# Optimization experiments

Measured on AMD Instinct MI355X. Metric: run time of the kernel, lower is better.

Reference implementation:

```python
import jax, jax.numpy as jnp
import numpy as np

DIM = 768
HEADS = 12
MLP_DIM = 3072
EPS = 1e-5


def setup_inputs() -> dict:
    key = jax.random.key(0)
    ks = jax.random.split(key, 10)
    s = lambda d: 1.0 / np.sqrt(d)
    return {
        "x": jax.random.normal(ks[0], (8, 1024, DIM), dtype=jnp.float32),
        "ln1_g": jnp.ones((DIM,), jnp.float32),
        "ln1_b": jnp.zeros((DIM,), jnp.float32),
        "w_qkv": jax.random.normal(ks[1], (DIM, 3 * DIM), jnp.float32) * s(DIM),
        "w_out": jax.random.normal(ks[2], (DIM, DIM), jnp.float32) * s(DIM),
        "b_out": jnp.zeros((DIM,), jnp.float32),
        "ln2_g": jnp.ones((DIM,), jnp.float32),
        "ln2_b": jnp.zeros((DIM,), jnp.float32),
        "w1": jax.random.normal(ks[3], (DIM, MLP_DIM), jnp.float32) * s(DIM),
        "b1": jnp.zeros((MLP_DIM,), jnp.float32),
        "w2": jax.random.normal(ks[4], (MLP_DIM, DIM), jnp.float32) * s(MLP_DIM),
        "b2": jnp.zeros((DIM,), jnp.float32),
    }


def _layernorm(x, g, b):
    mu = jnp.mean(x, axis=-1, keepdims=True)
    var = jnp.mean(jnp.square(x - mu), axis=-1, keepdims=True)
    return (x - mu) * jax.lax.rsqrt(var + EPS) * g + b


def _block(x, ln1_g, ln1_b, w_qkv, w_out, b_out, ln2_g, ln2_b, w1, b1, w2, b2):
    B, N, C = x.shape
    H = HEADS
    Dh = C // H
    scale = Dh ** -0.5
    # attention
    h = _layernorm(x, ln1_g, ln1_b)
    qkv = (h @ w_qkv).reshape(B, N, 3, H, Dh)
    q, k, v = qkv[:, :, 0], qkv[:, :, 1], qkv[:, :, 2]  # [B,N,H,Dh]
    attn = jnp.einsum("bnhd,bmhd->bhnm", q, k) * scale
    attn = jax.nn.softmax(attn, axis=-1)
    o = jnp.einsum("bhnm,bmhd->bnhd", attn, v).reshape(B, N, C)
    x = x + o @ w_out + b_out
    # mlp (exact erf GELU, matching torch nn.GELU default)
    h = _layernorm(x, ln2_g, ln2_b)
    h = jax.nn.gelu(h @ w1 + b1, approximate=False)
    x = x + h @ w2 + b2
    return x


def reference(x, ln1_g, ln1_b, w_qkv, w_out, b_out, ln2_g, ln2_b, w1, b1, w2, b2):
    return _block(x, ln1_g, ln1_b, w_qkv, w_out, b_out, ln2_g, ln2_b, w1, b1, w2, b2)
```

## Files before the change

### kernel.cpp

```cpp
#include <hip/hip_runtime.h>
#include <hip/hip_bf16.h>
#include <cstdint>

#define DIM 768
#define HEADS 12
#define DH 64
#define MLP_DIM 3072
#define ROWS 8192
#define SEQ 1024
#define PPAD 72

typedef __attribute__((ext_vector_type(8))) short bf16x8;
typedef __attribute__((ext_vector_type(4))) float f32x4;

typedef __attribute__((address_space(1))) void GV;
typedef __attribute__((address_space(3))) void SV;

__device__ inline void async16(const void* g, void* l) {
  __builtin_amdgcn_global_load_lds((GV*)(void*)g, (SV*)l, 16, 0, 0);
}

__device__ inline unsigned short f2b(float f) {
  union { float f; uint32_t u; } v; v.f = f;
  uint32_t u = v.u;
  return (unsigned short)((u + 0x7fffu + ((u >> 16) & 1u)) >> 16);
}

__device__ inline float gelu_f(float v) {
  float x = v * 0.70710678118654752f;
  float ax = fabsf(x);
  float t = 1.f / (1.f + 0.47047f * ax);
  float poly = t * (0.3480242f + t * (-0.0958798f + t * 0.7478556f));
  float erfv = 1.f - poly * __expf(-ax * ax);
  erfv = copysignf(erfv, x);
  return 0.5f * v * (1.f + erfv);
}

__global__ __launch_bounds__(256) void transpose_k(const float* __restrict__ in,
                                                   unsigned short* __restrict__ out,
                                                   int K, int N) {
  __shared__ float t[32][33];
  int tx = threadIdx.x & 31, ty = threadIdx.x >> 5;
  int bn = blockIdx.x * 32, bk = blockIdx.y * 32;
#pragma unroll
  for (int i = ty; i < 32; i += 8) t[i][tx] = in[(size_t)(bk + i) * N + bn + tx];
  __syncthreads();
#pragma unroll
  for (int i = ty; i < 32; i += 8) out[(size_t)(bn + i) * K + bk + tx] = f2b(t[tx][i]);
}

__global__ __launch_bounds__(256) void ln_k(const float* __restrict__ x,
                                            const float* __restrict__ g,
                                            const float* __restrict__ b,
                                            unsigned short* __restrict__ h) {
  int wave = threadIdx.x >> 6, lane = threadIdx.x & 63;
  int row = blockIdx.x * 4 + wave;
  const float4* xr = (const float4*)(x + (size_t)row * DIM);
  float4 v[3];
  float s = 0.f;
#pragma unroll
  for (int j = 0; j < 3; ++j) {
    v[j] = xr[lane + j * 64];
    s += (v[j].x + v[j].y) + (v[j].z + v[j].w);
  }
#pragma unroll
  for (int m = 1; m < 64; m <<= 1) s += __shfl_xor(s, m);
  float mu = s * (1.f / DIM);
  float vs = 0.f;
#pragma unroll
  for (int j = 0; j < 3; ++j) {
    float d0 = v[j].x - mu, d1 = v[j].y - mu, d2 = v[j].z - mu, d3 = v[j].w - mu;
    vs += (d0 * d0 + d1 * d1) + (d2 * d2 + d3 * d3);
  }
#pragma unroll
  for (int m = 1; m < 64; m <<= 1) vs += __shfl_xor(vs, m);
  float rstd = rsqrtf(vs * (1.f / DIM) + 1e-5f);
  const float4* g4 = (const float4*)g;
  const float4* b4 = (const float4*)b;
  unsigned short* hr = h + (size_t)row * DIM;
#pragma unroll
  for (int j = 0; j < 3; ++j) {
    int i = lane + j * 64;
    float4 gg = g4[i], bb = b4[i];
    float y0 = (v[j].x - mu) * rstd * gg.x + bb.x;
    float y1 = (v[j].y - mu) * rstd * gg.y + bb.y;
    float y2 = (v[j].z - mu) * rstd * gg.z + bb.z;
    float y3 = (v[j].w - mu) * rstd * gg.w + bb.w;
    uint2 pk;
    pk.x = (uint32_t)f2b(y0) | ((uint32_t)f2b(y1) << 16);
    pk.y = (uint32_t)f2b(y2) | ((uint32_t)f2b(y3) << 16);
    *(uint2*)(hr + i * 4) = pk;
  }
}

template <int MODE, int TM>
__global__ __launch_bounds__(256, 3) void gemm_k(
    const unsigned short* __restrict__ A, const unsigned short* __restrict__ Bt,
    int M, int N, int K,
    const float* __restrict__ bias, const float* __restrict__ resid,
    float* __restrict__ outf, unsigned short* __restrict__ outb) {
  constexpr int MI = (TM == 128) ? 4 : 2;
  __shared__ __align__(16) unsigned short As[2][TM * 64];
  __shared__ __align__(16) unsigned short Bs[2][128 * 64];
  int tid = threadIdx.x;
  int wave = tid >> 6, lane = tid & 63, lrow = lane & 15, qd = lane >> 4;
  int ntn = N >> 7;

  int nwg = gridDim.x;
  int wg = blockIdx.x;
  if ((nwg & 7) == 0) wg = (wg & 7) * (nwg >> 3) + (wg >> 3);

  int bm = (wg / ntn) * TM;
  int bn = (wg % ntn) << 7;
  int wm = (TM == 128) ? (wave >> 1) * 64 : (wave & 1) * 32;
  int wn = (TM == 128) ? (wave & 1) * 64 : (wave >> 1) * 64;

  f32x4 acc[MI][4];
#pragma unroll
  for (int i = 0; i < MI; ++i)
#pragma unroll
    for (int j = 0; j < 4; ++j) acc[i][j] = (f32x4){0.f, 0.f, 0.f, 0.f};

  int srow = tid >> 3;
  int c = (tid & 7) ^ (srow & 7);
  const char* gA = (const char*)(A + (size_t)(bm + srow) * K) + c * 16;
  const char* gB = (const char*)(Bt + (size_t)(bn + srow) * K) + c * 16;
  size_t rstep = (size_t)32 * K * 2;

  auto stage = [&](int kt, int buf) {
    size_t ko = (size_t)kt * 128;
    char* lA = (char*)(As[buf]) + tid * 16;
    char* lB = (char*)(Bs[buf]) + tid * 16;
#pragma unroll
    for (int j = 0; j < TM / 32; ++j) async16(gA + ko + j * rstep, lA + j * 4096);
#pragma unroll
    for (int j = 0; j < 4; ++j) async16(gB + ko + j * rstep, lB + j * 4096);
  };

  int nk = K >> 6;
  stage(0, 0);
  for (int kt = 0; kt < nk; ++kt) {
    asm volatile("s_waitcnt vmcnt(0)" ::: "memory");
    __syncthreads();
    if (kt + 1 < nk) stage(kt + 1, (kt + 1) & 1);
    const unsigned short* Asb = As[kt & 1];
    const unsigned short* Bsb = Bs[kt & 1];
#pragma unroll
    for (int s = 0; s < 2; ++s) {
      int q = s * 4 + qd;
      bf16x8 af[MI], bfr[4];
#pragma unroll
      for (int i = 0; i < MI; ++i) {
        int r = wm + i * 16 + lrow;
        af[i] = *(const bf16x8*)(Asb + r * 64 + ((q ^ (r & 7)) << 3));
      }
#pragma unroll
      for (int i = 0; i < 4; ++i) {
        int r = wn + i * 16 + lrow;
        bfr[i] = *(const bf16x8*)(Bsb + r * 64 + ((q ^ (r & 7)) << 3));
      }
#pragma unroll
      for (int mi = 0; mi < MI; ++mi)
#pragma unroll
        for (int ni = 0; ni < 4; ++ni)
          acc[mi][ni] = __builtin_amdgcn_mfma_f32_16x16x32_bf16(af[mi], bfr[ni], acc[mi][ni], 0, 0, 0);
    }
  }

#pragma unroll
  for (int mi = 0; mi < MI; ++mi)
#pragma unroll
    for (int ni = 0; ni < 4; ++ni)
#pragma unroll
      for (int r = 0; r < 4; ++r) {
        int row = bm + wm + mi * 16 + qd * 4 + r;
        int col = bn + wn + ni * 16 + lrow;
        float v = acc[mi][ni][r];
        if (MODE == 1) {
          v += bias[col] + resid[(size_t)row * 768 + col];
          outf[(size_t)row * 768 + col] = v;
        } else {
          v += bias[col];
          outb[(size_t)row * MLP_DIM + col] = f2b(gelu_f(v));
        }
      }
}

template <int MODE>
__global__ __launch_bounds__(256, 3) void gemm1b_k(
    const unsigned short* __restrict__ A, const unsigned short* __restrict__ Bt,
    int M, int N, int K,
    const float* __restrict__ bias,
    unsigned short* __restrict__ outb,
    unsigned short* __restrict__ Qb, unsigned short* __restrict__ Kb,
    unsigned short* __restrict__ Vt) {
  __shared__ __align__(16) unsigned short As[128 * 64];
  __shared__ __align__(16) unsigned short Bs[128 * 64];
  int tid = threadIdx.x;
  int wave = tid >> 6, lane = tid & 63, lrow = lane & 15, qd = lane >> 4;
  int ntn = N >> 7;

  int nwg = gridDim.x;
  int wg = blockIdx.x;
  if ((nwg & 7) == 0) wg = (wg & 7) * (nwg >> 3) + (wg >> 3);

  int bm = (wg / ntn) << 7;
  int bn = (wg % ntn) << 7;
  int wm = (wave >> 1) * 64;
  int wn = (wave & 1) * 64;

  f32x4 acc[4][4];
#pragma unroll
  for (int i = 0; i < 4; ++i)
#pragma unroll
    for (int j = 0; j < 4; ++j) acc[i][j] = (f32x4){0.f, 0.f, 0.f, 0.f};

  int srow = tid >> 3;
  int c = (tid & 7) ^ (srow & 7);
  const char* gA = (const char*)(A + (size_t)(bm + srow) * K) + c * 16;
  const char* gB = (const char*)(Bt + (size_t)(bn + srow) * K) + c * 16;
  size_t rstep = (size_t)32 * K * 2;

  auto stage = [&](int kt) {
    size_t ko = (size_t)kt * 128;
    char* lA = (char*)As + tid * 16;
    char* lB = (char*)Bs + tid * 16;
#pragma unroll
    for (int j = 0; j < 4; ++j) async16(gA + ko + j * rstep, lA + j * 4096);
#pragma unroll
    for (int j = 0; j < 4; ++j) async16(gB + ko + j * rstep, lB + j * 4096);
  };

  int nk = K >> 6;
  stage(0);
  for (int kt = 0; kt < nk; ++kt) {
    __syncthreads();
#pragma unroll
    for (int s = 0; s < 2; ++s) {
      int q = s * 4 + qd;
      bf16x8 af[4], bfr[4];
#pragma unroll
      for (int i = 0; i < 4; ++i) {
        int r = wm + i * 16 + lrow;
        af[i] = *(const bf16x8*)(As + r * 64 + ((q ^ (r & 7)) << 3));
      }
#pragma unroll
      for (int i = 0; i < 4; ++i) {
        int r = wn + i * 16 + lrow;
        bfr[i] = *(const bf16x8*)(Bs + r * 64 + ((q ^ (r & 7)) << 3));
      }
#pragma unroll
      for (int mi = 0; mi < 4; ++mi)
#pragma unroll
        for (int ni = 0; ni < 4; ++ni)
          acc[mi][ni] = __builtin_amdgcn_mfma_f32_16x16x32_bf16(af[mi], bfr[ni], acc[mi][ni], 0, 0, 0);
    }
    __syncthreads();
    if (kt + 1 < nk) stage(kt + 1);
  }

#pragma unroll
  for (int mi = 0; mi < 4; ++mi)
#pragma unroll
    for (int ni = 0; ni < 4; ++ni)
#pragma unroll
      for (int r = 0; r < 4; ++r) {
        int row = bm + wm + mi * 16 + qd * 4 + r;
        int col = bn + wn + ni * 16 + lrow;
        float v = acc[mi][ni][r];
        if (MODE == 0) {
          int which = col / 768;
          int rem = col - which * 768;
          int hh = rem >> 6, dh = rem & 63;
          int bb = row >> 10, n = row & 1023;
          size_t bh = (size_t)(bb * HEADS + hh);
          if (which == 0) {
            Qb[(bh * SEQ + n) * DH + dh] = f2b(v * 0.125f);
          } else if (which == 1) {
            Kb[(bh * SEQ + n) * DH + (((dh >> 3) ^ (n & 7)) << 3) + (dh & 7)] = f2b(v);
          } else {
            Vt[(bh * DH + dh) * SEQ + (n & ~63) +
               ((((n >> 3) & 7) ^ (dh & 7)) << 3) + (n & 7)] = f2b(v);
          }
        } else {
          v += bias[col];
          outb[(size_t)row * MLP_DIM + col] = f2b(gelu_f(v));
        }
      }
}

__global__ __launch_bounds__(256, 3) void attn_k(const unsigned short* __restrict__ Qb,
                                                 const unsigned short* __restrict__ Kb,
                                                 const unsigned short* __restrict__ Vt,
                                                 unsigned short* __restrict__ o) {
  __shared__ __align__(16) unsigned short Ks[2][64 * 64];
  __shared__ __align__(16) unsigned short Vs[2][64 * 64];
  __shared__ __align__(16) unsigned short Pa[4][32 * PPAD];
  int tid = threadIdx.x;
  int wave = tid >> 6, lane = tid & 63;
  int lrow = lane & 15, qd = lane >> 4;
  int bh = blockIdx.x % 96;
  int qt = blockIdx.x / 96;
  int b = bh / HEADS, hh = bh % HEADS;
  const unsigned short* Qh = Qb + (size_t)bh * SEQ * DH;
  const char* Kh = (const char*)(Kb + (size_t)bh * SEQ * DH);
  const char* Vh = (const char*)(Vt + (size_t)bh * DH * SEQ);
  int qw = qt * 128 + wave * 32;

  bf16x8 qf[2][2];
#pragma unroll
  for (int qs = 0; qs < 2; ++qs)
#pragma unroll
    for (int hf = 0; hf < 2; ++hf)
      qf[qs][hf] = *(const bf16x8*)(Qh + (qw + qs * 16 + lrow) * DH + hf * 32 + qd * 8);

  f32x4 oacc[2][4];
#pragma unroll
  for (int qs = 0; qs < 2; ++qs)
#pragma unroll
    for (int d = 0; d < 4; ++d) oacc[qs][d] = (f32x4){0.f, 0.f, 0.f, 0.f};
  float li[2] = {0.f, 0.f};
  unsigned short* Pw = Pa[wave];

  auto stage = [&](int t, int buf) {
    const char* kbase = Kh + (size_t)t * 8192;
    char* kd = (char*)Ks[buf];
    async16(kbase + tid * 16, kd + tid * 16);
    async16(kbase + 4096 + tid * 16, kd + 4096 + tid * 16);
    const char* vbase = Vh + (size_t)t * 128;
    char* vd = (char*)Vs[buf];
    async16(vbase + (size_t)(tid >> 3) * 2048 + (tid & 7) * 16, vd + tid * 16);
    async16(vbase + (size_t)((tid >> 3) + 32) * 2048 + (tid & 7) * 16, vd + 4096 + tid * 16);
  };

  stage(0, 0);
  for (int t = 0; t < 16; ++t) {
    asm volatile("s_waitcnt vmcnt(0)" ::: "memory");
    __syncthreads();
    if (t < 15) stage(t + 1, (t + 1) & 1);
    const unsigned short* Kst = Ks[t & 1];
    const unsigned short* Vst = Vs[t & 1];

    f32x4 st[4][2];
#pragma unroll
    for (int kt = 0; kt < 4; ++kt) {
      int krow = kt * 16 + lrow;
      int ksw = krow & 7;
      const unsigned short* Kr = Kst + krow * 64;
      bf16x8 k0 = *(const bf16x8*)(Kr + ((qd ^ ksw) << 3));
      bf16x8 k1 = *(const bf16x8*)(Kr + (((qd + 4) ^ ksw) << 3));
#pragma unroll
      for (int qs = 0; qs < 2; ++qs) {
        f32x4 z = (f32x4){0.f, 0.f, 0.f, 0.f};
        z = __builtin_amdgcn_mfma_f32_16x16x32_bf16(k0, qf[qs][0], z, 0, 0, 0);
        z = __builtin_amdgcn_mfma_f32_16x16x32_bf16(k1, qf[qs][1], z, 0, 0, 0);
        st[kt][qs] = z;
      }
    }

#pragma unroll
    for (int kt = 0; kt < 4; ++kt)
#pragma unroll
      for (int qs = 0; qs < 2; ++qs) {
        float p0 = __expf(st[kt][qs][0]);
        float p1 = __expf(st[kt][qs][1]);
        float p2 = __expf(st[kt][qs][2]);
        float p3 = __expf(st[kt][qs][3]);
        li[qs] += (p0 + p1) + (p2 + p3);
        uint2 pk;
        pk.x = (uint32_t)f2b(p0) | ((uint32_t)f2b(p1) << 16);
        pk.y = (uint32_t)f2b(p2) | ((uint32_t)f2b(p3) << 16);
        *(uint2*)(Pw + (qs * 16 + lrow) * PPAD + kt * 16 + qd * 4) = pk;
      }
    asm volatile("s_waitcnt lgkmcnt(0)" ::: "memory");

    bf16x8 ap[2][2];
#pragma unroll
    for (int qs = 0; qs < 2; ++qs)
#pragma unroll
      for (int kh = 0; kh < 2; ++kh)
        ap[qs][kh] = *(const bf16x8*)(Pw + (qs * 16 + lrow) * PPAD + kh * 32 + qd * 8);

#pragma unroll
    for (int ds = 0; ds < 4; ++ds) {
      int vrow = ds * 16 + lrow;
      int vsw = vrow & 7;
      const unsigned short* Vr = Vst + vrow * 64;
      bf16x8 v0 = *(const bf16x8*)(Vr + ((qd ^ vsw) << 3));
      bf16x8 v1 = *(const bf16x8*)(Vr + (((4 + qd) ^ vsw) << 3));
#pragma unroll
      for (int qs = 0; qs < 2; ++qs) {
        oacc[qs][ds] = __builtin_amdgcn_mfma_f32_16x16x32_bf16(ap[qs][0], v0, oacc[qs][ds], 0, 0, 0);
        oacc[qs][ds] = __builtin_amdgcn_mfma_f32_16x16x32_bf16(ap[qs][1], v1, oacc[qs][ds], 0, 0, 0);
      }
    }
  }

#pragma unroll
  for (int qs = 0; qs < 2; ++qs) {
    li[qs] += __shfl_xor(li[qs], 16);
    li[qs] += __shfl_xor(li[qs], 32);
  }

#pragma unroll
  for (int qs = 0; qs < 2; ++qs)
#pragma unroll
    for (int r = 0; r < 4; ++r) {
      float inv = 1.f / __shfl(li[qs], qd * 4 + r);
      int n = qw + qs * 16 + qd * 4 + r;
#pragma unroll
      for (int ds = 0; ds < 4; ++ds) {
        int dh = ds * 16 + lrow;
        o[((size_t)(b * SEQ + n)) * DIM + hh * DH + dh] = f2b(oacc[qs][ds][r] * inv);
      }
    }
}

extern "C" void kernel_launch(void* const* d_in, const int* in_sizes, int n_in,
                              void* d_out, int out_size, void* d_ws, size_t ws_size,
                              hipStream_t stream) {
  const float* x     = (const float*)d_in[0];
  const float* ln1_g = (const float*)d_in[1];
  const float* ln1_b = (const float*)d_in[2];
  const float* w_qkv = (const float*)d_in[3];
  const float* w_out = (const float*)d_in[4];
  const float* b_out = (const float*)d_in[5];
  const float* ln2_g = (const float*)d_in[6];
  const float* ln2_b = (const float*)d_in[7];
  const float* w1    = (const float*)d_in[8];
  const float* b1    = (const float*)d_in[9];
  const float* w2    = (const float*)d_in[10];
  const float* b2    = (const float*)d_in[11];

  char* ws = (char*)d_ws;
  unsigned short* wqkvT = (unsigned short*)(ws + 0);
  unsigned short* woutT = (unsigned short*)(ws + 3538944);
  unsigned short* w1T   = (unsigned short*)(ws + 4718592);
  unsigned short* w2T   = (unsigned short*)(ws + 9437184);
  float*          x2    = (float*)(ws + 14155776);
  unsigned short* h     = (unsigned short*)(ws + 39321600);
  char* big = ws + 51904512;
  unsigned short* Qb = (unsigned short*)(big);
  unsigned short* Kb = (unsigned short*)(big + 12582912);
  unsigned short* Vt = (unsigned short*)(big + 25165824);
  unsigned short* ob = (unsigned short*)(big + 37748736);
  unsigned short* am = (unsigned short*)(big);

  transpose_k<<<dim3(72, 24), 256, 0, stream>>>(w_qkv, wqkvT, 768, 2304);
  transpose_k<<<dim3(24, 24), 256, 0, stream>>>(w_out, woutT, 768, 768);
  transpose_k<<<dim3(96, 24), 256, 0, stream>>>(w1, w1T, 768, 3072);
  transpose_k<<<dim3(24, 96), 256, 0, stream>>>(w2, w2T, 3072, 768);

  ln_k<<<2048, 256, 0, stream>>>(x, ln1_g, ln1_b, h);
  gemm1b_k<0><<<64 * 18, 256, 0, stream>>>(h, wqkvT, ROWS, 2304, 768,
                                           nullptr, nullptr, Qb, Kb, Vt);
  attn_k<<<768, 256, 0, stream>>>(Qb, Kb, Vt, ob);
  gemm_k<1, 64><<<128 * 6, 256, 0, stream>>>(ob, woutT, ROWS, 768, 768,
                                             b_out, x, x2, nullptr);
  ln_k<<<2048, 256, 0, stream>>>(x2, ln2_g, ln2_b, h);
  gemm1b_k<2><<<64 * 24, 256, 0, stream>>>(h, w1T, ROWS, 3072, 768,
                                           b1, am, nullptr, nullptr, nullptr);
  gemm_k<1, 64><<<128 * 6, 256, 0, stream>>>(am, w2T, ROWS, 768, 3072,
                                             b2, x2, (float*)d_out, nullptr);
}
```

Before: 356.9 us.

## Use 8-wave 256x128 GEMM tiles and single-buffered 128x64 tiles for projections

The QKV and MLP-up GEMMs move to a 512-thread kernel with 256x128 output tiles, so each B tile is reused across more rows. The N=768 GEMMs (out-proj, MLP-down) change from double-buffered 64x128 tiles to single-buffered 128x64 tiles with occupancy hint 4. Dropping double buffering gives up load/compute overlap inside a workgroup in exchange for less LDS and more resident workgroups. The larger tiles also mean fewer workgroups per GEMM, which may hurt wave balance across CUs.

```diff
diff --git a/kernel.cpp b/kernel.cpp
--- a/kernel.cpp
+++ b/kernel.cpp
@@ -93,33 +93,35 @@
   }
 }
 
-template <int MODE, int TM>
-__global__ __launch_bounds__(256, 3) void gemm_k(
+template <int MODE, int BN>
+__global__ __launch_bounds__(256, 4) void gemm1b_k(
     const unsigned short* __restrict__ A, const unsigned short* __restrict__ Bt,
     int M, int N, int K,
     const float* __restrict__ bias, const float* __restrict__ resid,
-    float* __restrict__ outf, unsigned short* __restrict__ outb) {
-  constexpr int MI = (TM == 128) ? 4 : 2;
-  __shared__ __align__(16) unsigned short As[2][TM * 64];
-  __shared__ __align__(16) unsigned short Bs[2][128 * 64];
+    float* __restrict__ outf, unsigned short* __restrict__ outb,
+    unsigned short* __restrict__ Qb, unsigned short* __restrict__ Kb,
+    unsigned short* __restrict__ Vt) {
+  constexpr int NI = BN / 32;
+  __shared__ __align__(16) unsigned short As[128 * 64];
+  __shared__ __align__(16) unsigned short Bs[BN * 64];
   int tid = threadIdx.x;
   int wave = tid >> 6, lane = tid & 63, lrow = lane & 15, qd = lane >> 4;
-  int ntn = N >> 7;
+  int ntn = N / BN;
 
   int nwg = gridDim.x;
   int wg = blockIdx.x;
   if ((nwg & 7) == 0) wg = (wg & 7) * (nwg >> 3) + (wg >> 3);
 
-  int bm = (wg / ntn) * TM;
-  int bn = (wg % ntn) << 7;
-  int wm = (TM == 128) ? (wave >> 1) * 64 : (wave & 1) * 32;
-  int wn = (TM == 128) ? (wave & 1) * 64 : (wave >> 1) * 64;
-
-  f32x4 acc[MI][4];
-#pragma unroll
-  for (int i = 0; i < MI; ++i)
-#pragma unroll
-    for (int j = 0; j < 4; ++j) acc[i][j] = (f32x4){0.f, 0.f, 0.f, 0.f};
+  int bm = (wg / ntn) << 7;
+  int bn = (wg % ntn) * BN;
+  int wm = (wave >> 1) * 64;
+  int wn = (wave & 1) * (BN / 2);
+
+  f32x4 acc[4][NI];
+#pragma unroll
+  for (int i = 0; i < 4; ++i)
+#pragma unroll
+    for (int j = 0; j < NI; ++j) acc[i][j] = (f32x4){0.f, 0.f, 0.f, 0.f};
 
   int srow = tid >> 3;
   int c = (tid & 7) ^ (srow & 7);
@@ -127,50 +129,48 @@
   const char* gB = (const char*)(Bt + (size_t)(bn + srow) * K) + c * 16;
   size_t rstep = (size_t)32 * K * 2;
 
-  auto stage = [&](int kt, int buf) {
+  auto stage = [&](int kt) {
     size_t ko = (size_t)kt * 128;
-    char* lA = (char*)(As[buf]) + tid * 16;
-    char* lB = (char*)(Bs[buf]) + tid * 16;
-#pragma unroll
-    for (int j = 0; j < TM / 32; ++j) async16(gA + ko + j * rstep, lA + j * 4096);
-#pragma unroll
-    for (int j = 0; j < 4; ++j) async16(gB + ko + j * rstep, lB + j * 4096);
+    char* lA = (char*)As + tid * 16;
+    char* lB = (char*)Bs + tid * 16;
+#pragma unroll
+    for (int j = 0; j < 4; ++j) async16(gA + ko + j * rstep, lA + j * 4096);
+#pragma unroll
+    for (int j = 0; j < BN / 32; ++j) async16(gB + ko + j * rstep, lB + j * 4096);
   };
 
   int nk = K >> 6;
-  stage(0, 0);
+  stage(0);
   for (int kt = 0; kt < nk; ++kt) {
-    asm volatile("s_waitcnt vmcnt(0)" ::: "memory");
     __syncthreads();
-    if (kt + 1 < nk) stage(kt + 1, (kt + 1) & 1);
-    const unsigned short* Asb = As[kt & 1];
-    const unsigned short* Bsb = Bs[kt & 1];
 #pragma unroll
     for (int s = 0; s < 2; ++s) {
       int q = s * 4 + qd;
-      bf16x8 af[MI], bfr[4];
-#pragma unroll
-      for (int i = 0; i < MI; ++i) {
+      bf16x8 af[4], bfr[NI];
+#pragma unroll
+      for (int i = 0; i < 4; ++i) {
         int r = wm + i * 16 + lrow;
-        af[i] = *(const bf16x8*)(Asb + r * 64 + ((q ^ (r & 7)) << 3));
-      }
-#pragma unroll
-      for (int i = 0; i < 4; ++i) {
+        af[i] = *(const bf16x8*)(As + r * 64 + ((q ^ (r & 7)) << 3));
+      }
+#pragma unroll
+      for (int i = 0; i < NI; ++i) {
         int r = wn + i * 16 + lrow;
-        bfr[i] = *(const bf16x8*)(Bsb + r * 64 + ((q ^ (r & 7)) << 3));
-      }
-#pragma unroll
-      for (int mi = 0; mi < MI; ++mi)
-#pragma unroll
-        for (int ni = 0; ni < 4; ++ni)
+        bfr[i] = *(const bf16x8*)(Bs + r * 64 + ((q ^ (r & 7)) << 3));
+      }
+#pragma unroll
+      for (int mi = 0; mi < 4; ++mi)
+#pragma unroll
+        for (int ni = 0; ni < NI; ++ni)
           acc[mi][ni] = __builtin_amdgcn_mfma_f32_16x16x32_bf16(af[mi], bfr[ni], acc[mi][ni], 0, 0, 0);
     }
-  }
-
-#pragma unroll
-  for (int mi = 0; mi < MI; ++mi)
-#pragma unroll
-    for (int ni = 0; ni < 4; ++ni)
+    __syncthreads();
+    if (kt + 1 < nk) stage(kt + 1);
+  }
+
+#pragma unroll
+  for (int mi = 0; mi < 4; ++mi)
+#pragma unroll
+    for (int ni = 0; ni < NI; ++ni)
 #pragma unroll
       for (int r = 0; r < 4; ++r) {
         int row = bm + wm + mi * 16 + qd * 4 + r;
@@ -187,14 +187,14 @@
 }
 
 template <int MODE>
-__global__ __launch_bounds__(256, 3) void gemm1b_k(
+__global__ __launch_bounds__(512, 6) void gemm8w_k(
     const unsigned short* __restrict__ A, const unsigned short* __restrict__ Bt,
     int M, int N, int K,
     const float* __restrict__ bias,
     unsigned short* __restrict__ outb,
     unsigned short* __restrict__ Qb, unsigned short* __restrict__ Kb,
     unsigned short* __restrict__ Vt) {
-  __shared__ __align__(16) unsigned short As[128 * 64];
+  __shared__ __align__(16) unsigned short As[256 * 64];
   __shared__ __align__(16) unsigned short Bs[128 * 64];
   int tid = threadIdx.x;
   int wave = tid >> 6, lane = tid & 63, lrow = lane & 15, qd = lane >> 4;
@@ -204,10 +204,10 @@
   int wg = blockIdx.x;
   if ((nwg & 7) == 0) wg = (wg & 7) * (nwg >> 3) + (wg >> 3);
 
-  int bm = (wg / ntn) << 7;
+  int bm = (wg / ntn) << 8;
   int bn = (wg % ntn) << 7;
-  int wm = (wave >> 1) * 64;
-  int wn = (wave & 1) * 64;
+  int wm = (wave & 3) * 64;
+  int wn = (wave >> 2) * 64;
 
   f32x4 acc[4][4];
 #pragma unroll
@@ -219,16 +219,16 @@
   int c = (tid & 7) ^ (srow & 7);
   const char* gA = (const char*)(A + (size_t)(bm + srow) * K) + c * 16;
   const char* gB = (const char*)(Bt + (size_t)(bn + srow) * K) + c * 16;
-  size_t rstep = (size_t)32 * K * 2;
+  size_t rstep = (size_t)64 * K * 2;
 
   auto stage = [&](int kt) {
     size_t ko = (size_t)kt * 128;
     char* lA = (char*)As + tid * 16;
     char* lB = (char*)Bs + tid * 16;
 #pragma unroll
-    for (int j = 0; j < 4; ++j) async16(gA + ko + j * rstep, lA + j * 4096);
-#pragma unroll
-    for (int j = 0; j < 4; ++j) async16(gB + ko + j * rstep, lB + j * 4096);
+    for (int j = 0; j < 4; ++j) async16(gA + ko + j * rstep, lA + j * 8192);
+#pragma unroll
+    for (int j = 0; j < 2; ++j) async16(gB + ko + j * rstep, lB + j * 8192);
   };
 
   int nk = K >> 6;
@@ -452,14 +452,14 @@
   transpose_k<<<dim3(24, 96), 256, 0, stream>>>(w2, w2T, 3072, 768);
 
   ln_k<<<2048, 256, 0, stream>>>(x, ln1_g, ln1_b, h);
-  gemm1b_k<0><<<64 * 18, 256, 0, stream>>>(h, wqkvT, ROWS, 2304, 768,
+  gemm8w_k<0><<<32 * 18, 512, 0, stream>>>(h, wqkvT, ROWS, 2304, 768,
                                            nullptr, nullptr, Qb, Kb, Vt);
   attn_k<<<768, 256, 0, stream>>>(Qb, Kb, Vt, ob);
-  gemm_k<1, 64><<<128 * 6, 256, 0, stream>>>(ob, woutT, ROWS, 768, 768,
-                                             b_out, x, x2, nullptr);
+  gemm1b_k<1, 64><<<64 * 12, 256, 0, stream>>>(ob, woutT, ROWS, 768, 768,
+                                               b_out, x, x2, nullptr, nullptr, nullptr, nullptr);
   ln_k<<<2048, 256, 0, stream>>>(x2, ln2_g, ln2_b, h);
-  gemm1b_k<2><<<64 * 24, 256, 0, stream>>>(h, w1T, ROWS, 3072, 768,
+  gemm8w_k<2><<<32 * 24, 512, 0, stream>>>(h, w1T, ROWS, 3072, 768,
                                            b1, am, nullptr, nullptr, nullptr);
-  gemm_k<1, 64><<<128 * 6, 256, 0, stream>>>(am, w2T, ROWS, 768, 3072,
-                                             b2, x2, (float*)d_out, nullptr);
-}
+  gemm1b_k<1, 64><<<64 * 12, 256, 0, stream>>>(am, w2T, ROWS, 768, 3072,
+                                               b2, x2, (float*)d_out, nullptr, nullptr, nullptr, nullptr);
+}
```

Result: slower. 843.1 us (+136.2%).

## Merge weight transposes with first layernorm; retile output GEMMs to 128x64

Applied to the files above, without the earlier changes.

Merges the four weight-transpose launches and the first layernorm into a single prep kernel, so fewer launches are issued. Replaces the 64x128-tile output-projection and MLP-down GEMM with a new 128x64-tile kernel, where each wave computes 64x32 instead of 32x64. It also raises the minimum occupancy hint for gemm1b_k from 3 to 4 blocks, which may force fewer registers and cause spills.

```diff
diff --git a/kernel.cpp b/kernel.cpp
--- a/kernel.cpp
+++ b/kernel.cpp
@@ -36,25 +36,11 @@
   return 0.5f * v * (1.f + erfv);
 }
 
-__global__ __launch_bounds__(256) void transpose_k(const float* __restrict__ in,
-                                                   unsigned short* __restrict__ out,
-                                                   int K, int N) {
-  __shared__ float t[32][33];
-  int tx = threadIdx.x & 31, ty = threadIdx.x >> 5;
-  int bn = blockIdx.x * 32, bk = blockIdx.y * 32;
-#pragma unroll
-  for (int i = ty; i < 32; i += 8) t[i][tx] = in[(size_t)(bk + i) * N + bn + tx];
-  __syncthreads();
-#pragma unroll
-  for (int i = ty; i < 32; i += 8) out[(size_t)(bn + i) * K + bk + tx] = f2b(t[tx][i]);
-}
-
-__global__ __launch_bounds__(256) void ln_k(const float* __restrict__ x,
-                                            const float* __restrict__ g,
-                                            const float* __restrict__ b,
-                                            unsigned short* __restrict__ h) {
-  int wave = threadIdx.x >> 6, lane = threadIdx.x & 63;
-  int row = blockIdx.x * 4 + wave;
+__device__ inline void ln_row(const float* __restrict__ x,
+                              const float* __restrict__ g,
+                              const float* __restrict__ b,
+                              unsigned short* __restrict__ h,
+                              int row, int lane) {
   const float4* xr = (const float4*)(x + (size_t)row * DIM);
   float4 v[3];
   float s = 0.f;
@@ -93,101 +79,46 @@
   }
 }
 
-template <int MODE, int TM>
-__global__ __launch_bounds__(256, 3) void gemm_k(
-    const unsigned short* __restrict__ A, const unsigned short* __restrict__ Bt,
-    int M, int N, int K,
-    const float* __restrict__ bias, const float* __restrict__ resid,
-    float* __restrict__ outf, unsigned short* __restrict__ outb) {
-  constexpr int MI = (TM == 128) ? 4 : 2;
-  __shared__ __align__(16) unsigned short As[2][TM * 64];
-  __shared__ __align__(16) unsigned short Bs[2][128 * 64];
-  int tid = threadIdx.x;
-  int wave = tid >> 6, lane = tid & 63, lrow = lane & 15, qd = lane >> 4;
-  int ntn = N >> 7;
-
-  int nwg = gridDim.x;
-  int wg = blockIdx.x;
-  if ((nwg & 7) == 0) wg = (wg & 7) * (nwg >> 3) + (wg >> 3);
-
-  int bm = (wg / ntn) * TM;
-  int bn = (wg % ntn) << 7;
-  int wm = (TM == 128) ? (wave >> 1) * 64 : (wave & 1) * 32;
-  int wn = (TM == 128) ? (wave & 1) * 64 : (wave >> 1) * 64;
-
-  f32x4 acc[MI][4];
-#pragma unroll
-  for (int i = 0; i < MI; ++i)
-#pragma unroll
-    for (int j = 0; j < 4; ++j) acc[i][j] = (f32x4){0.f, 0.f, 0.f, 0.f};
-
-  int srow = tid >> 3;
-  int c = (tid & 7) ^ (srow & 7);
-  const char* gA = (const char*)(A + (size_t)(bm + srow) * K) + c * 16;
-  const char* gB = (const char*)(Bt + (size_t)(bn + srow) * K) + c * 16;
-  size_t rstep = (size_t)32 * K * 2;
-
-  auto stage = [&](int kt, int buf) {
-    size_t ko = (size_t)kt * 128;
-    char* lA = (char*)(As[buf]) + tid * 16;
-    char* lB = (char*)(Bs[buf]) + tid * 16;
-#pragma unroll
-    for (int j = 0; j < TM / 32; ++j) async16(gA + ko + j * rstep, lA + j * 4096);
-#pragma unroll
-    for (int j = 0; j < 4; ++j) async16(gB + ko + j * rstep, lB + j * 4096);
-  };
-
-  int nk = K >> 6;
-  stage(0, 0);
-  for (int kt = 0; kt < nk; ++kt) {
-    asm volatile("s_waitcnt vmcnt(0)" ::: "memory");
-    __syncthreads();
-    if (kt + 1 < nk) stage(kt + 1, (kt + 1) & 1);
-    const unsigned short* Asb = As[kt & 1];
-    const unsigned short* Bsb = Bs[kt & 1];
-#pragma unroll
-    for (int s = 0; s < 2; ++s) {
-      int q = s * 4 + qd;
-      bf16x8 af[MI], bfr[4];
-#pragma unroll
-      for (int i = 0; i < MI; ++i) {
-        int r = wm + i * 16 + lrow;
-        af[i] = *(const bf16x8*)(Asb + r * 64 + ((q ^ (r & 7)) << 3));
-      }
-#pragma unroll
-      for (int i = 0; i < 4; ++i) {
-        int r = wn + i * 16 + lrow;
-        bfr[i] = *(const bf16x8*)(Bsb + r * 64 + ((q ^ (r & 7)) << 3));
-      }
-#pragma unroll
-      for (int mi = 0; mi < MI; ++mi)
-#pragma unroll
-        for (int ni = 0; ni < 4; ++ni)
-          acc[mi][ni] = __builtin_amdgcn_mfma_f32_16x16x32_bf16(af[mi], bfr[ni], acc[mi][ni], 0, 0, 0);
-    }
-  }
-
-#pragma unroll
-  for (int mi = 0; mi < MI; ++mi)
-#pragma unroll
-    for (int ni = 0; ni < 4; ++ni)
-#pragma unroll
-      for (int r = 0; r < 4; ++r) {
-        int row = bm + wm + mi * 16 + qd * 4 + r;
-        int col = bn + wn + ni * 16 + lrow;
-        float v = acc[mi][ni][r];
-        if (MODE == 1) {
-          v += bias[col] + resid[(size_t)row * 768 + col];
-          outf[(size_t)row * 768 + col] = v;
-        } else {
-          v += bias[col];
-          outb[(size_t)row * MLP_DIM + col] = f2b(gelu_f(v));
-        }
-      }
+__global__ __launch_bounds__(256) void ln_k(const float* __restrict__ x,
+                                            const float* __restrict__ g,
+                                            const float* __restrict__ b,
+                                            unsigned short* __restrict__ h) {
+  int wave = threadIdx.x >> 6, lane = threadIdx.x & 63;
+  ln_row(x, g, b, h, blockIdx.x * 4 + wave, lane);
+}
+
+__global__ __launch_bounds__(256) void prep_k(
+    const float* __restrict__ w_qkv, const float* __restrict__ w_out,
+    const float* __restrict__ w1, const float* __restrict__ w2,
+    const float* __restrict__ x,
+    const float* __restrict__ ln1_g, const float* __restrict__ ln1_b,
+    unsigned short* __restrict__ wqkvT, unsigned short* __restrict__ woutT,
+    unsigned short* __restrict__ w1T, unsigned short* __restrict__ w2T,
+    unsigned short* __restrict__ h) {
+  __shared__ float t[32][33];
+  int id = blockIdx.x;
+  if (id < 2048) {
+    int wave = threadIdx.x >> 6, lane = threadIdx.x & 63;
+    ln_row(x, ln1_g, ln1_b, h, id * 4 + wave, lane);
+    return;
+  }
+  id -= 2048;
+  const float* in; unsigned short* out; int K, N, bx, by;
+  if (id < 1728)        { in = w_qkv; out = wqkvT; K = 768;  N = 2304; bx = id % 72; by = id / 72; }
+  else if (id < 2304)   { id -= 1728; in = w_out; out = woutT; K = 768;  N = 768;  bx = id % 24; by = id / 24; }
+  else if (id < 4608)   { id -= 2304; in = w1;    out = w1T;   K = 768;  N = 3072; bx = id % 96; by = id / 96; }
+  else                  { id -= 4608; in = w2;    out = w2T;   K = 3072; N = 768;  bx = id % 24; by = id / 24; }
+  int tx = threadIdx.x & 31, ty = threadIdx.x >> 5;
+  int bn = bx * 32, bk = by * 32;
+#pragma unroll
+  for (int i = ty; i < 32; i += 8) t[i][tx] = in[(size_t)(bk + i) * N + bn + tx];
+  __syncthreads();
+#pragma unroll
+  for (int i = ty; i < 32; i += 8) out[(size_t)(bn + i) * K + bk + tx] = f2b(t[tx][i]);
 }
 
 template <int MODE>
-__global__ __launch_bounds__(256, 3) void gemm1b_k(
+__global__ __launch_bounds__(256, 4) void gemm1b_k(
     const unsigned short* __restrict__ A, const unsigned short* __restrict__ Bt,
     int M, int N, int K,
     const float* __restrict__ bias,
@@ -289,6 +220,91 @@
       }
 }
 
+__global__ __launch_bounds__(256, 3) void gemm2b_k(
+    const unsigned short* __restrict__ A, const unsigned short* __restrict__ Bt,
+    int M, int N, int K,
+    const float* __restrict__ bias, const float* __restrict__ resid,
+    float* __restrict__ outf) {
+  __shared__ __align__(16) unsigned short As[2][128 * 64];
+  __shared__ __align__(16) unsigned short Bs[2][64 * 64];
+  int tid = threadIdx.x;
+  int wave = tid >> 6, lane = tid & 63, lrow = lane & 15, qd = lane >> 4;
+  int ntn = N >> 6;
+
+  int nwg = gridDim.x;
+  int wg = blockIdx.x;
+  if ((nwg & 7) == 0) wg = (wg & 7) * (nwg >> 3) + (wg >> 3);
+
+  int bm = (wg / ntn) << 7;
+  int bn = (wg % ntn) << 6;
+  int wm = (wave >> 1) * 64;
+  int wn = (wave & 1) * 32;
+
+  f32x4 acc[4][2];
+#pragma unroll
+  for (int i = 0; i < 4; ++i)
+#pragma unroll
+    for (int j = 0; j < 2; ++j) acc[i][j] = (f32x4){0.f, 0.f, 0.f, 0.f};
+
+  int srow = tid >> 3;
+  int c = (tid & 7) ^ (srow & 7);
+  const char* gA = (const char*)(A + (size_t)(bm + srow) * K) + c * 16;
+  const char* gB = (const char*)(Bt + (size_t)(bn + srow) * K) + c * 16;
+  size_t rstep = (size_t)32 * K * 2;
+
+  auto stage = [&](int kt, int buf) {
+    size_t ko = (size_t)kt * 128;
+    char* lA = (char*)(As[buf]) + tid * 16;
+    char* lB = (char*)(Bs[buf]) + tid * 16;
+#pragma unroll
+    for (int j = 0; j < 4; ++j) async16(gA + ko + j * rstep, lA + j * 4096);
+#pragma unroll
+    for (int j = 0; j < 2; ++j) async16(gB + ko + j * rstep, lB + j * 4096);
+  };
+
+  int nk = K >> 6;
+  stage(0, 0);
+  for (int kt = 0; kt < nk; ++kt) {
+    asm volatile("s_waitcnt vmcnt(0)" ::: "memory");
+    __syncthreads();
+    if (kt + 1 < nk) stage(kt + 1, (kt + 1) & 1);
+    const unsigned short* Asb = As[kt & 1];
+    const unsigned short* Bsb = Bs[kt & 1];
+#pragma unroll
+    for (int s = 0; s < 2; ++s) {
+      int q = s * 4 + qd;
+      bf16x8 af[4], bfr[2];
+#pragma unroll
+      for (int i = 0; i < 4; ++i) {
+        int r = wm + i * 16 + lrow;
+        af[i] = *(const bf16x8*)(Asb + r * 64 + ((q ^ (r & 7)) << 3));
+      }
+#pragma unroll
+      for (int i = 0; i < 2; ++i) {
+        int r = wn + i * 16 + lrow;
+        bfr[i] = *(const bf16x8*)(Bsb + r * 64 + ((q ^ (r & 7)) << 3));
+      }
+#pragma unroll
+      for (int mi = 0; mi < 4; ++mi)
+#pragma unroll
+        for (int ni = 0; ni < 2; ++ni)
+          acc[mi][ni] = __builtin_amdgcn_mfma_f32_16x16x32_bf16(af[mi], bfr[ni], acc[mi][ni], 0, 0, 0);
+    }
+  }
+
+#pragma unroll
+  for (int mi = 0; mi < 4; ++mi)
+#pragma unroll
+    for (int ni = 0; ni < 2; ++ni)
+#pragma unroll
+      for (int r = 0; r < 4; ++r) {
+        int row = bm + wm + mi * 16 + qd * 4 + r;
+        int col = bn + wn + ni * 16 + lrow;
+        float v = acc[mi][ni][r] + bias[col] + resid[(size_t)row * 768 + col];
+        outf[(size_t)row * 768 + col] = v;
+      }
+}
+
 __global__ __launch_bounds__(256, 3) void attn_k(const unsigned short* __restrict__ Qb,
                                                  const unsigned short* __restrict__ Kb,
                                                  const unsigned short* __restrict__ Vt,
@@ -446,20 +462,16 @@
   unsigned short* ob = (unsigned short*)(big + 37748736);
   unsigned short* am = (unsigned short*)(big);
 
-  transpose_k<<<dim3(72, 24), 256, 0, stream>>>(w_qkv, wqkvT, 768, 2304);
-  transpose_k<<<dim3(24, 24), 256, 0, stream>>>(w_out, woutT, 768, 768);
-  transpose_k<<<dim3(96, 24), 256, 0, stream>>>(w1, w1T, 768, 3072);
-  transpose_k<<<dim3(24, 96), 256, 0, stream>>>(w2, w2T, 3072, 768);
-
-  ln_k<<<2048, 256, 0, stream>>>(x, ln1_g, ln1_b, h);
+  prep_k<<<8960, 256, 0, stream>>>(w_qkv, w_out, w1, w2, x, ln1_g, ln1_b,
+                                   wqkvT, woutT, w1T, w2T, h);
   gemm1b_k<0><<<64 * 18, 256, 0, stream>>>(h, wqkvT, ROWS, 2304, 768,
                                            nullptr, nullptr, Qb, Kb, Vt);
   attn_k<<<768, 256, 0, stream>>>(Qb, Kb, Vt, ob);
-  gemm_k<1, 64><<<128 * 6, 256, 0, stream>>>(ob, woutT, ROWS, 768, 768,
-                                             b_out, x, x2, nullptr);
+  gemm2b_k<<<64 * 12, 256, 0, stream>>>(ob, woutT, ROWS, 768, 768,
+                                        b_out, x, x2);
   ln_k<<<2048, 256, 0, stream>>>(x2, ln2_g, ln2_b, h);
   gemm1b_k<2><<<64 * 24, 256, 0, stream>>>(h, w1T, ROWS, 3072, 768,
                                            b1, am, nullptr, nullptr, nullptr);
-  gemm_k<1, 64><<<128 * 6, 256, 0, stream>>>(am, w2T, ROWS, 768, 3072,
-                                             b2, x2, (float*)d_out, nullptr);
-}
+  gemm2b_k<<<64 * 12, 256, 0, stream>>>(am, w2T, ROWS, 768, 3072,
+                                        b2, x2, (float*)d_out);
+}
```

Result: faster. 345.9 us (-3.1%).
